# Optimization experiments

Hardware: AMD Instinct MI355X
Metric: run time of the kernel (lower is better)

The kernel has to match this reference:

```python
import jax, jax.numpy as jnp
import numpy as np

DIM = 384
HEADS = 6
HEAD_DIM = DIM // HEADS
MLP_DIM = int(DIM * 4.0)
EPS = 1e-5


def layer_norm(x, g, b):
    mu = jnp.mean(x, axis=-1, keepdims=True)
    var = jnp.mean(jnp.square(x - mu), axis=-1, keepdims=True)
    return (x - mu) * jax.lax.rsqrt(var + EPS) * g + b


def setup_inputs() -> dict:
    key = jax.random.key(0)
    ks = jax.random.split(key, 12)
    s = 0.02
    return {
        "x": jax.random.normal(ks[0], (8, 2048, DIM), dtype=jnp.float32),
        "ln1_g": jnp.ones((DIM,), jnp.float32),
        "ln1_b": jnp.zeros((DIM,), jnp.float32),
        "qkv_w": jax.random.normal(ks[1], (DIM, 3 * DIM), jnp.float32) * s,
        "qkv_b": jnp.zeros((3 * DIM,), jnp.float32),
        "proj_w": jax.random.normal(ks[2], (DIM, DIM), jnp.float32) * s,
        "proj_b": jnp.zeros((DIM,), jnp.float32),
        "ln2_g": jnp.ones((DIM,), jnp.float32),
        "ln2_b": jnp.zeros((DIM,), jnp.float32),
        "fc1_w": jax.random.normal(ks[3], (DIM, MLP_DIM), jnp.float32) * s,
        "fc1_b": jnp.zeros((MLP_DIM,), jnp.float32),
        "fc2_w": jax.random.normal(ks[4], (MLP_DIM, DIM), jnp.float32) * s,
        "fc2_b": jnp.zeros((DIM,), jnp.float32),
    }


def reference(x, ln1_g, ln1_b, qkv_w, qkv_b, proj_w, proj_b,
              ln2_g, ln2_b, fc1_w, fc1_b, fc2_w, fc2_b):
    B, N, C = x.shape
    # --- attention ---
    h = layer_norm(x, ln1_g, ln1_b)
    qkv = h @ qkv_w + qkv_b  # [B,N,3C]
    qkv = qkv.reshape(B, N, 3, HEADS, HEAD_DIM)
    q, k, v = jnp.moveaxis(qkv, 2, 0)  # each [B,N,H,D]
    scale = HEAD_DIM ** -0.5
    attn = jnp.einsum('bnhd,bmhd->bhnm', q, k) * scale  # [B,H,N,N]
    attn = jax.nn.softmax(attn, axis=-1)
    o = jnp.einsum('bhnm,bmhd->bnhd', attn, v).reshape(B, N, C)
    x = x + o @ proj_w + proj_b
    # --- mlp ---
    h = layer_norm(x, ln2_g, ln2_b)
    h = jax.nn.gelu(h @ fc1_w + fc1_b, approximate=False)
    x = x + h @ fc2_w + fc2_b
    return x
```

## Files before the change

### kernel.cpp

```cpp
#include <hip/hip_runtime.h>
#include <hip/hip_bf16.h>

#define DIM   384
#define SEQ   2048
#define BATCH 8
#define NHEAD 6
#define HD    64
#define MLPD  1536
#define MTOT  (BATCH*SEQ)

typedef __attribute__((ext_vector_type(8))) short bf16x8;
typedef __attribute__((ext_vector_type(4))) float f32x4;

static __device__ __forceinline__ float bf2f(unsigned short u){
    union { float f; unsigned int i; } v; v.i = ((unsigned int)u) << 16; return v.f;
}
static __device__ __forceinline__ unsigned short f2bf(float f){
    union { float f; unsigned int i; } v; v.f = f;
    unsigned int r = v.i + 0x7fffu + ((v.i >> 16) & 1u);
    return (unsigned short)(r >> 16);
}
static __device__ __forceinline__ unsigned int asu(float f){
    union { float f; unsigned int i; } v; v.f = f; return v.i;
}
static __device__ __forceinline__ void gload_lds16(const unsigned short* g, unsigned short* l){
    __builtin_amdgcn_global_load_lds(
        (__attribute__((address_space(1))) void*)(g),
        (__attribute__((address_space(3))) void*)(l), 16, 0, 0);
}
static __device__ __forceinline__ void barx(){
    asm volatile("" ::: "memory");
    __builtin_amdgcn_s_barrier();
    asm volatile("" ::: "memory");
}
#define WAITVM(N) asm volatile("s_waitcnt vmcnt(" #N ")" ::: "memory")

static __device__ __forceinline__ int xcd_lin(){
    return (blockIdx.x & 7) * ((int)gridDim.x >> 3) + ((int)blockIdx.x >> 3);
}

__global__ __launch_bounds__(256) void wt_all_kernel(
    const float* __restrict__ qkv_w, const float* __restrict__ proj_w,
    const float* __restrict__ fc1_w, const float* __restrict__ fc2_w,
    unsigned short* __restrict__ o_qkv, unsigned short* __restrict__ o_prj,
    unsigned short* __restrict__ o_fc1, unsigned short* __restrict__ o_fc2)
{
    __shared__ float tile[64][68];
    int bid = blockIdx.x;
    const float* W; unsigned short* Wt; int K, N, tk, tn;
    if (bid < 108)      { W = qkv_w; Wt = o_qkv; K = 384;  N = 1152; tk = bid/18;        tn = bid%18; }
    else if (bid < 144) { W = proj_w; Wt = o_prj; K = 384;  N = 384;  tk = (bid-108)/6;  tn = (bid-108)%6; }
    else if (bid < 288) { W = fc1_w; Wt = o_fc1; K = 384;  N = 1536; tk = (bid-144)/24; tn = (bid-144)%24; }
    else                { W = fc2_w; Wt = o_fc2; K = 1536; N = 384;  tk = (bid-288)/6;  tn = (bid-288)%6; }
    int t = threadIdx.x;
    int lr = t >> 4, lc = (t & 15) * 4;
#pragma unroll
    for (int p = 0; p < 4; p++){
        float4 v = *(const float4*)(W + (size_t)(tk*64 + p*16 + lr) * N + tn*64 + lc);
        *(float4*)&tile[p*16 + lr][lc] = v;
    }
    __syncthreads();
    int n = t >> 2, k0 = (t & 3) * 16;
    unsigned int w[8];
#pragma unroll
    for (int i = 0; i < 8; i++)
        w[i] = (unsigned int)f2bf(tile[k0 + 2*i][n]) | ((unsigned int)f2bf(tile[k0 + 2*i + 1][n]) << 16);
    unsigned short* dst = Wt + (size_t)(tn*64 + n) * K + tk*64 + k0;
    *(uint4*)(dst)     = make_uint4(w[0], w[1], w[2], w[3]);
    *(uint4*)(dst + 8) = make_uint4(w[4], w[5], w[6], w[7]);
}

__global__ __launch_bounds__(256) void ln_kernel(const float* __restrict__ x,
                                                 const float* __restrict__ g,
                                                 const float* __restrict__ b,
                                                 unsigned short* __restrict__ out){
    int row  = blockIdx.x * 4 + (threadIdx.x >> 6);
    int lane = threadIdx.x & 63;
    const float* xr = x + (size_t)row * DIM;
    float v[6];
#pragma unroll
    for (int p = 0; p < 3; p++){
        float2 t = *(const float2*)(xr + lane * 2 + p * 128);
        v[2*p] = t.x; v[2*p+1] = t.y;
    }
    float s = 0.f, sq = 0.f;
#pragma unroll
    for (int i = 0; i < 6; i++){ s += v[i]; sq += v[i] * v[i]; }
#pragma unroll
    for (int off = 1; off < 64; off <<= 1){
        s  += __shfl_xor(s, off);
        sq += __shfl_xor(sq, off);
    }
    float mu   = s * (1.0f / DIM);
    float var  = sq * (1.0f / DIM) - mu * mu;
    float rstd = rsqrtf(var + 1e-5f);
    unsigned short* orow = out + (size_t)row * DIM;
#pragma unroll
    for (int p = 0; p < 3; p++){
        int c = lane * 2 + p * 128;
        float h0 = (v[2*p]   - mu) * rstd * g[c]   + b[c];
        float h1 = (v[2*p+1] - mu) * rstd * g[c+1] + b[c+1];
        unsigned int pk = (unsigned int)f2bf(h0) | ((unsigned int)f2bf(h1) << 16);
        *(unsigned int*)(orow + c) = pk;
    }
}

template<int EPI, int NC>
__global__ __launch_bounds__(128, 3) void gemm_kernel(
    const unsigned short* __restrict__ A, const unsigned short* __restrict__ Bt,
    const float* __restrict__ bias, int K, int N,
    const float* __restrict__ resid, float* __restrict__ outf,
    unsigned short* __restrict__ outb,
    unsigned short* __restrict__ qb, unsigned short* __restrict__ kb2,
    unsigned short* __restrict__ vb)
{
    __shared__ __align__(16) unsigned short smem[64*64 + 128*64];
    unsigned short* As = smem;
    unsigned short* Bs = smem + 64*64;
    int t = threadIdx.x;
    int wid = t >> 6, lane = t & 63, quad = lane >> 4, l15 = lane & 15;
    int lin = xcd_lin();
    int row0 = (lin / NC) * 64, col0 = (lin % NC) * 128;
    int sr = lane >> 3, sc = lane & 7;
    int scl = (sc ^ sr) * 8;

    const unsigned short* Ab = A  + (size_t)row0 * K;
    const unsigned short* Bb = Bt + (size_t)col0 * K;

    f32x4 acc[2][8];
    f32x4 zz = {0.f, 0.f, 0.f, 0.f};
#pragma unroll
    for (int i = 0; i < 2; i++)
#pragma unroll
        for (int j = 0; j < 8; j++) acc[i][j] = zz;

    for (int k0 = 0; k0 < K; k0 += 64){
        __syncthreads();
#pragma unroll
        for (int jj = 0; jj < 4; jj++){
            int rb = wid * 32 + jj * 8;
            gload_lds16(Ab + (size_t)(rb + sr) * K + k0 + scl, &As[rb * 64]);
        }
#pragma unroll
        for (int jj = 0; jj < 8; jj++){
            int rb = wid * 64 + jj * 8;
            gload_lds16(Bb + (size_t)(rb + sr) * K + k0 + scl, &Bs[rb * 64]);
        }
        __syncthreads();
#pragma unroll
        for (int kk = 0; kk < 2; kk++){
            bf16x8 af[2], bf[8];
#pragma unroll
            for (int i = 0; i < 2; i++){
                int r = wid*32 + i*16 + l15;
                af[i] = *(const bf16x8*)&As[r * 64 + (((kk*4 + quad) ^ (l15 & 7)) * 8)];
            }
#pragma unroll
            for (int j = 0; j < 8; j++){
                int r = j*16 + l15;
                bf[j] = *(const bf16x8*)&Bs[r * 64 + (((kk*4 + quad) ^ (l15 & 7)) * 8)];
            }
#pragma unroll
            for (int i = 0; i < 2; i++)
#pragma unroll
                for (int j = 0; j < 8; j++)
                    acc[i][j] = __builtin_amdgcn_mfma_f32_16x16x32_bf16(af[i], bf[j], acc[i][j], 0, 0, 0);
        }
    }

    if (EPI == 0 && col0 >= 768){
        __syncthreads();
        unsigned short* T = smem;
#pragma unroll
        for (int i = 0; i < 2; i++)
#pragma unroll
            for (int j = 0; j < 8; j++){
                int gcl = j*16 + l15;
                float bia = bias[col0 + gcl];
                int nsl0 = wid*32 + i*16 + quad*4;
#pragma unroll
                for (int r = 0; r < 4; r++)
                    T[gcl * 72 + nsl0 + r] = f2bf(acc[i][j][r] + bia);
            }
        __syncthreads();
        int rem = (col0 - 768) + t;
        int head = rem >> 6, d = rem & 63;
        int bidx = row0 >> 11, ns0 = row0 & 2047;
        unsigned short* dst = vb + ((size_t)((bidx * NHEAD + head) * 64 + d)) * SEQ + ns0;
        const unsigned short* src = T + t * 72;
#pragma unroll
        for (int m = 0; m < 8; m++)
            *(uint4*)(dst + m*8) = *(const uint4*)(src + m*8);
        return;
    }

#pragma unroll
    for (int i = 0; i < 2; i++){
#pragma unroll
        for (int j = 0; j < 8; j++){
            int gr0 = row0 + wid*32 + i*16 + quad*4;
            int gc  = col0 + j*16 + l15;
            float bia = bias[gc];
#pragma unroll
            for (int r = 0; r < 4; r++){
                int gr = gr0 + r;
                float val = acc[i][j][r] + bia;
                if (EPI == 1){
                    outf[(size_t)gr * N + gc] = resid[(size_t)gr * N + gc] + val;
                } else if (EPI == 2){
                    float u = val * (1.0f + 0.044715f * val * val);
                    float e = __builtin_amdgcn_exp2f(u * 2.3025851f);
                    outb[(size_t)gr * N + gc] = f2bf(val * e / (e + 1.0f));
                } else {
                    int trip = gc / 384, remq = gc - trip * 384;
                    int head = remq >> 6, d = remq & 63;
                    int bidx = gr >> 11, ns = gr & 2047;
                    size_t off = ((size_t)(bidx * NHEAD + head) * SEQ + ns) * 64 + d;
                    unsigned short* dstp = (trip == 0) ? qb : kb2;
                    dstp[off] = f2bf(val);
                }
            }
        }
    }
}

template<int LOFF>
static __device__ __forceinline__ void attn_tile(
    const bf16x8 (&qf)[2][2], const bf16x8& ones,
    const unsigned short* const (&kf_ptr)[4][2],
    const unsigned short* const (&vf_ptr)[2][4],
    const unsigned short* const (&pf_ptr)[2][2],
    uint2* const (&pw_ptr)[2][4],
    f32x4 (&sacc)[2], f32x4 (&oacc)[2][4])
{
    const f32x4 zz = {0.f, 0.f, 0.f, 0.f};
    f32x4 st[2][4];
#pragma unroll
    for (int n = 0; n < 4; n++){
        bf16x8 kf0 = *(const bf16x8*)(kf_ptr[n][0] + LOFF);
        bf16x8 kf1 = *(const bf16x8*)(kf_ptr[n][1] + LOFF);
#pragma unroll
        for (int h = 0; h < 2; h++){
            f32x4 z = __builtin_amdgcn_mfma_f32_16x16x32_bf16(kf0, qf[h][0], zz, 0, 0, 0);
            st[h][n] = __builtin_amdgcn_mfma_f32_16x16x32_bf16(kf1, qf[h][1], z, 0, 0, 0);
        }
    }
#pragma unroll
    for (int h = 0; h < 2; h++){
#pragma unroll
        for (int n = 0; n < 4; n++){
            float p0 = __builtin_amdgcn_exp2f(st[h][n][0]);
            float p1 = __builtin_amdgcn_exp2f(st[h][n][1]);
            float p2 = __builtin_amdgcn_exp2f(st[h][n][2]);
            float p3 = __builtin_amdgcn_exp2f(st[h][n][3]);
            unsigned int w0 = __builtin_amdgcn_perm(asu(p1), asu(p0), 0x07060302u);
            unsigned int w1 = __builtin_amdgcn_perm(asu(p3), asu(p2), 0x07060302u);
            *pw_ptr[h][n] = make_uint2(w0, w1);
        }
    }
    asm volatile("s_waitcnt lgkmcnt(0)" ::: "memory");
#pragma unroll
    for (int c = 0; c < 2; c++){
        bf16x8 pf[2];
#pragma unroll
        for (int h = 0; h < 2; h++)
            pf[h] = *(const bf16x8*)pf_ptr[c][h];
        sacc[0] = __builtin_amdgcn_mfma_f32_16x16x32_bf16(ones, pf[0], sacc[0], 0, 0, 0);
        sacc[1] = __builtin_amdgcn_mfma_f32_16x16x32_bf16(ones, pf[1], sacc[1], 0, 0, 0);
#pragma unroll
        for (int dn = 0; dn < 4; dn++){
            bf16x8 vf = *(const bf16x8*)(vf_ptr[c][dn] + LOFF);
            oacc[0][dn] = __builtin_amdgcn_mfma_f32_16x16x32_bf16(vf, pf[0], oacc[0][dn], 0, 0, 0);
            oacc[1][dn] = __builtin_amdgcn_mfma_f32_16x16x32_bf16(vf, pf[1], oacc[1][dn], 0, 0, 0);
        }
    }
}

__global__ __launch_bounds__(256, 3) void attn_kernel(const unsigned short* __restrict__ Q,
                                                      const unsigned short* __restrict__ Kb,
                                                      const unsigned short* __restrict__ Vt,
                                                      unsigned short* __restrict__ O){
    __shared__ __align__(16) unsigned short smem[16384 + 4*2048];

    int lin = xcd_lin();
    int qt = lin & 15, bh = lin >> 4;
    int t = threadIdx.x, wid = t >> 6, lane = t & 63, quad = lane >> 4, l15 = lane & 15;
    int l7 = l15 & 7;
    int q0 = qt * 128 + wid * 32;
    const unsigned short* Qp = Q  + (size_t)bh * SEQ * 64;
    const unsigned short* Kp = Kb + (size_t)bh * SEQ * 64;
    const unsigned short* Vp = Vt + (size_t)bh * 64 * SEQ;
    int sr = lane >> 3, sc = lane & 7;
    int scl = (sc ^ sr) * 8;

    const float QSCALE = 0.125f * 1.44269504f;
    bf16x8 qf[2][2];
#pragma unroll
    for (int h = 0; h < 2; h++){
#pragma unroll
        for (int c = 0; c < 2; c++){
            union { uint4 u; unsigned short s[8]; } cv;
            cv.u = *(const uint4*)(Qp + (size_t)(q0 + h*16 + l15) * 64 + c * 32 + quad * 8);
            bf16x8 f;
#pragma unroll
            for (int j = 0; j < 8; j++) f[j] = (short)f2bf(bf2f(cv.s[j]) * QSCALE);
            qf[h][c] = f;
        }
    }

    bf16x8 ones;
#pragma unroll
    for (int j = 0; j < 8; j++) ones[j] = (short)0x3F80;

    f32x4 oacc[2][4], sacc[2];
    f32x4 zz = {0.f, 0.f, 0.f, 0.f};
#pragma unroll
    for (int h = 0; h < 2; h++){
        sacc[h] = zz;
#pragma unroll
        for (int dn = 0; dn < 4; dn++) oacc[h][dn] = zz;
    }
    unsigned short* P = &smem[16384 + wid * 2048];

    const unsigned short* kf_ptr[4][2];
#pragma unroll
    for (int n = 0; n < 4; n++){
        int kv = n * 16 + l15;
        kf_ptr[n][0] = &smem[kv * 64 + ((quad       ^ (kv & 7)) * 8)];
        kf_ptr[n][1] = &smem[kv * 64 + (((4 + quad) ^ (kv & 7)) * 8)];
    }
    const unsigned short* vf_ptr[2][4];
#pragma unroll
    for (int c = 0; c < 2; c++)
#pragma unroll
        for (int dn = 0; dn < 4; dn++){
            int d = dn * 16 + l15;
            vf_ptr[c][dn] = &smem[4096 + d * 64 + (((c*4 + quad) ^ (d & 7)) * 8)];
        }
    const unsigned short* pf_ptr[2][2];
#pragma unroll
    for (int c = 0; c < 2; c++)
#pragma unroll
        for (int h = 0; h < 2; h++)
            pf_ptr[c][h] = P + (h*16 + l15) * 64 + (((c*4 + quad) ^ l7) * 8);
    uint2* pw_ptr[2][4];
#pragma unroll
    for (int h = 0; h < 2; h++)
#pragma unroll
        for (int n = 0; n < 4; n++){
            int qloc = h * 16 + l15;
            int chunk = n * 2 + (quad >> 1);
            pw_ptr[h][n] = (uint2*)(P + qloc * 64 + ((chunk ^ l7) * 8) + (quad & 1) * 4);
        }
    const unsigned short* kstage[2];
    const unsigned short* vstage[2];
    unsigned short* klds[2];
    unsigned short* vlds[2];
#pragma unroll
    for (int jj = 0; jj < 2; jj++){
        int rb = wid * 16 + jj * 8;
        kstage[jj] = Kp + (size_t)(rb + sr) * 64 + scl;
        vstage[jj] = Vp + (size_t)(rb + sr) * SEQ + scl;
        klds[jj] = &smem[rb * 64];
        vlds[jj] = &smem[4096 + rb * 64];
    }

#define AISSUE(BOFF) do { \
    _Pragma("unroll") \
    for (int jj = 0; jj < 2; jj++){ \
        gload_lds16(kstage[jj], klds[jj] + (BOFF)); \
        gload_lds16(vstage[jj], vlds[jj] + (BOFF)); \
        kstage[jj] += 64 * 64; \
        vstage[jj] += 64; \
    } } while(0)

    AISSUE(0);
    for (int p = 0; p < SEQ/128 - 1; p++){
        AISSUE(8192);
        WAITVM(4);
        barx();
        attn_tile<0>(qf, ones, kf_ptr, vf_ptr, pf_ptr, pw_ptr, sacc, oacc);
        barx();
        AISSUE(0);
        WAITVM(4);
        barx();
        attn_tile<8192>(qf, ones, kf_ptr, vf_ptr, pf_ptr, pw_ptr, sacc, oacc);
        barx();
    }
    AISSUE(8192);
    WAITVM(4);
    barx();
    attn_tile<0>(qf, ones, kf_ptr, vf_ptr, pf_ptr, pw_ptr, sacc, oacc);
    barx();
    WAITVM(0);
    barx();
    attn_tile<8192>(qf, ones, kf_ptr, vf_ptr, pf_ptr, pw_ptr, sacc, oacc);
#undef AISSUE

    int b = bh / NHEAD, hh = bh - b * NHEAD;
#pragma unroll
    for (int h = 0; h < 2; h++){
        float rd = 1.0f / sacc[h][0];
        size_t row = (size_t)(b * SEQ + q0 + h*16 + l15);
#pragma unroll
        for (int dn = 0; dn < 4; dn++){
            float v0 = oacc[h][dn][0] * rd, v1 = oacc[h][dn][1] * rd;
            float v2 = oacc[h][dn][2] * rd, v3 = oacc[h][dn][3] * rd;
            unsigned int w0 = (unsigned int)f2bf(v0) | ((unsigned int)f2bf(v1) << 16);
            unsigned int w1 = (unsigned int)f2bf(v2) | ((unsigned int)f2bf(v3) << 16);
            *(uint2*)(O + row * DIM + hh * 64 + dn * 16 + quad * 4) = make_uint2(w0, w1);
        }
    }
}

extern "C" void kernel_launch(void* const* d_in, const int* in_sizes, int n_in,
                              void* d_out, int out_size, void* d_ws, size_t ws_size,
                              hipStream_t stream){
    const float* x      = (const float*)d_in[0];
    const float* ln1_g  = (const float*)d_in[1];
    const float* ln1_b  = (const float*)d_in[2];
    const float* qkv_w  = (const float*)d_in[3];
    const float* qkv_b  = (const float*)d_in[4];
    const float* proj_w = (const float*)d_in[5];
    const float* proj_b = (const float*)d_in[6];
    const float* ln2_g  = (const float*)d_in[7];
    const float* ln2_b  = (const float*)d_in[8];
    const float* fc1_w  = (const float*)d_in[9];
    const float* fc1_b  = (const float*)d_in[10];
    const float* fc2_w  = (const float*)d_in[11];
    const float* fc2_b  = (const float*)d_in[12];
    float* out = (float*)d_out;

    char* p = (char*)d_ws;
    auto take = [&](size_t n){ char* r = p; p += (n + 255) & ~(size_t)255; return r; };
    unsigned short* wt_qkv = (unsigned short*)take((size_t)1152 * 384 * 2);
    unsigned short* wt_prj = (unsigned short*)take((size_t)384 * 384 * 2);
    unsigned short* wt_fc1 = (unsigned short*)take((size_t)1536 * 384 * 2);
    unsigned short* wt_fc2 = (unsigned short*)take((size_t)384 * 1536 * 2);
    unsigned short* rbig   = (unsigned short*)take((size_t)MTOT * 4 * DIM * 2);
    unsigned short* h2     = (unsigned short*)take((size_t)MTOT * DIM * 2);
    float*          x1     = (float*)take((size_t)MTOT * DIM * 4);

    unsigned short* h1     = rbig;
    unsigned short* qb     = rbig + (size_t)MTOT * DIM;
    unsigned short* kb     = qb   + (size_t)MTOT * DIM;
    unsigned short* vb     = kb   + (size_t)MTOT * DIM;
    unsigned short* attn_o = rbig;
    unsigned short* hm     = rbig;

    wt_all_kernel<<<dim3(432), 256, 0, stream>>>(qkv_w, proj_w, fc1_w, fc2_w,
                                                 wt_qkv, wt_prj, wt_fc1, wt_fc2);
    ln_kernel<<<dim3(MTOT/4), 256, 0, stream>>>(x, ln1_g, ln1_b, h1);
    gemm_kernel<0,9><<<dim3(2304), 128, 0, stream>>>(h1, wt_qkv, qkv_b, 384, 1152,
                                                     nullptr, nullptr, nullptr, qb, kb, vb);
    attn_kernel<<<dim3(768), 256, 0, stream>>>(qb, kb, vb, attn_o);
    gemm_kernel<1,3><<<dim3(768), 128, 0, stream>>>(attn_o, wt_prj, proj_b, 384, 384,
                                                    x, x1, nullptr, nullptr, nullptr, nullptr);
    ln_kernel<<<dim3(MTOT/4), 256, 0, stream>>>(x1, ln2_g, ln2_b, h2);
    gemm_kernel<2,12><<<dim3(3072), 128, 0, stream>>>(h2, wt_fc1, fc1_b, 384, 1536,
                                                      nullptr, nullptr, hm, nullptr, nullptr, nullptr);
    gemm_kernel<1,3><<<dim3(768), 128, 0, stream>>>(hm, wt_fc2, fc2_b, 1536, 384,
                                                    x1, out, nullptr, nullptr, nullptr, nullptr);
}
```

Baseline: 268.9 us.

## Load GEMM A fragments directly to registers and add MFMA priority hints in attention

In the GEMM, the A tile is no longer staged through LDS. Each lane now reads its bf16x8 A fragments straight from global memory into registers, which shrinks shared memory and raises the launch-bounds occupancy target from 3 to 4. The attention tile also wraps its MFMA sections in s_setprio raises so those waves get issue priority over others doing the exp work. The trade-off is uncoalesced, row-strided global reads of A per lane and higher register pressure under the tighter occupancy bound.

```diff
diff --git a/kernel.cpp b/kernel.cpp
--- a/kernel.cpp
+++ b/kernel.cpp
@@ -106,7 +106,7 @@
 }
 
 template<int EPI, int NC>
-__global__ __launch_bounds__(128, 3) void gemm_kernel(
+__global__ __launch_bounds__(128, 4) void gemm_kernel(
     const unsigned short* __restrict__ A, const unsigned short* __restrict__ Bt,
     const float* __restrict__ bias, int K, int N,
     const float* __restrict__ resid, float* __restrict__ outf,
@@ -114,9 +114,8 @@
     unsigned short* __restrict__ qb, unsigned short* __restrict__ kb2,
     unsigned short* __restrict__ vb)
 {
-    __shared__ __align__(16) unsigned short smem[64*64 + 128*64];
-    unsigned short* As = smem;
-    unsigned short* Bs = smem + 64*64;
+    __shared__ __align__(16) unsigned short smem[128 * 72];
+    unsigned short* Bs = smem;
     int t = threadIdx.x;
     int wid = t >> 6, lane = t & 63, quad = lane >> 4, l15 = lane & 15;
     int lin = xcd_lin();
@@ -124,8 +123,11 @@
     int sr = lane >> 3, sc = lane & 7;
     int scl = (sc ^ sr) * 8;
 
-    const unsigned short* Ab = A  + (size_t)row0 * K;
     const unsigned short* Bb = Bt + (size_t)col0 * K;
+    const unsigned short* arow[2];
+#pragma unroll
+    for (int i = 0; i < 2; i++)
+        arow[i] = A + (size_t)(row0 + wid*32 + i*16 + l15) * K + quad * 8;
 
     f32x4 acc[2][8];
     f32x4 zz = {0.f, 0.f, 0.f, 0.f};
@@ -136,25 +138,21 @@
 
     for (int k0 = 0; k0 < K; k0 += 64){
         __syncthreads();
-#pragma unroll
-        for (int jj = 0; jj < 4; jj++){
-            int rb = wid * 32 + jj * 8;
-            gload_lds16(Ab + (size_t)(rb + sr) * K + k0 + scl, &As[rb * 64]);
-        }
 #pragma unroll
         for (int jj = 0; jj < 8; jj++){
             int rb = wid * 64 + jj * 8;
             gload_lds16(Bb + (size_t)(rb + sr) * K + k0 + scl, &Bs[rb * 64]);
         }
+        bf16x8 af[2][2];
+#pragma unroll
+        for (int kk = 0; kk < 2; kk++)
+#pragma unroll
+            for (int i = 0; i < 2; i++)
+                af[kk][i] = *(const bf16x8*)(arow[i] + k0 + kk * 32);
         __syncthreads();
 #pragma unroll
         for (int kk = 0; kk < 2; kk++){
-            bf16x8 af[2], bf[8];
-#pragma unroll
-            for (int i = 0; i < 2; i++){
-                int r = wid*32 + i*16 + l15;
-                af[i] = *(const bf16x8*)&As[r * 64 + (((kk*4 + quad) ^ (l15 & 7)) * 8)];
-            }
+            bf16x8 bf[8];
 #pragma unroll
             for (int j = 0; j < 8; j++){
                 int r = j*16 + l15;
@@ -164,7 +162,7 @@
             for (int i = 0; i < 2; i++)
 #pragma unroll
                 for (int j = 0; j < 8; j++)
-                    acc[i][j] = __builtin_amdgcn_mfma_f32_16x16x32_bf16(af[i], bf[j], acc[i][j], 0, 0, 0);
+                    acc[i][j] = __builtin_amdgcn_mfma_f32_16x16x32_bf16(af[kk][i], bf[j], acc[i][j], 0, 0, 0);
         }
     }
 
@@ -235,6 +233,7 @@
 {
     const f32x4 zz = {0.f, 0.f, 0.f, 0.f};
     f32x4 st[2][4];
+    __builtin_amdgcn_s_setprio(1);
 #pragma unroll
     for (int n = 0; n < 4; n++){
         bf16x8 kf0 = *(const bf16x8*)(kf_ptr[n][0] + LOFF);
@@ -245,6 +244,7 @@
             st[h][n] = __builtin_amdgcn_mfma_f32_16x16x32_bf16(kf1, qf[h][1], z, 0, 0, 0);
         }
     }
+    __builtin_amdgcn_s_setprio(0);
 #pragma unroll
     for (int h = 0; h < 2; h++){
 #pragma unroll
@@ -259,6 +259,7 @@
         }
     }
     asm volatile("s_waitcnt lgkmcnt(0)" ::: "memory");
+    __builtin_amdgcn_s_setprio(1);
 #pragma unroll
     for (int c = 0; c < 2; c++){
         bf16x8 pf[2];
@@ -274,6 +275,7 @@
             oacc[1][dn] = __builtin_amdgcn_mfma_f32_16x16x32_bf16(vf, pf[1], oacc[1][dn], 0, 0, 0);
         }
     }
+    __builtin_amdgcn_s_setprio(0);
 }
 
 __global__ __launch_bounds__(256, 3) void attn_kernel(const unsigned short* __restrict__ Q,
```

Measured after the change: 336.2 us. +25.1%, slower.
